# Kernel optimization log

Measured on AMD Instinct MI355X. Metric: run time of the kernel, lower is better.

Reference implementation:

```python
import jax, jax.numpy as jnp
import numpy as np


def setup_inputs() -> dict:
    key = jax.random.key(0)
    k1, k2, k3 = jax.random.split(key, 3)
    B, N = 4096, 1024
    src = jax.random.normal(k1, (B, 3, N), dtype=jnp.float32)
    src_corr = jax.random.normal(k2, (B, 3, N), dtype=jnp.float32)
    weight = jax.random.uniform(k3, (B, 1, N), dtype=jnp.float32)
    return {"src": src, "src_corr": src_corr, "weight": weight}


def reference(src, src_corr, weight):
    # src, src_corr: (B, 3, N); weight: (B, 1, N)
    wsum = weight.sum(axis=2, keepdims=True)                      # (B,1,1)
    src2 = (src * weight).sum(axis=2, keepdims=True) / wsum       # (B,3,1) weighted centroid
    corr2 = (src_corr * weight).sum(axis=2, keepdims=True) / wsum  # (B,3,1)
    src_c = src - src2
    corr_c = src_corr - corr2
    # weighted 3x3 covariance H = (src_c * w) @ corr_c^T
    H = jnp.einsum('bin,bjn->bij', src_c * weight, corr_c)        # (B,3,3)
    u, s, vh = jnp.linalg.svd(H, full_matrices=False)
    v = jnp.swapaxes(vh, -1, -2)                                   # (B,3,3)
    ut = jnp.swapaxes(u, -1, -2)
    det = jnp.linalg.det(v @ ut)                                   # (B,)
    # R = v @ diag(1,1,det) @ u^T  -> scale last column of v by det
    v_adj = v.at[:, :, 2].multiply(det[:, None])
    R = v_adj @ ut                                                 # (B,3,3)
    t = -jnp.matmul(R, src2) + corr2                               # (B,3,1)
    return R, t
```

## Files before the change

kernel.cpp:

```cpp
#include <hip/hip_runtime.h>
#include <math.h>


__global__ __launch_bounds__(256, 3) void wsvd_fused(
    const float* __restrict__ src, const float* __restrict__ corr,
    const float* __restrict__ wgt, float* __restrict__ out, int B)
{
    const int gtid = blockIdx.x * 256 + threadIdx.x;
    const int b = gtid >> 6;
    const int lane = gtid & 63;

    const float4* W4 = reinterpret_cast<const float4*>(wgt  + (size_t)b * 1024);
    const float4* S4 = reinterpret_cast<const float4*>(src  + (size_t)b * 3072);
    const float4* C4 = reinterpret_cast<const float4*>(corr + (size_t)b * 3072);

    float4 wv0 = W4[lane],        wv1 = W4[lane + 64],
           wv2 = W4[lane + 128],  wv3 = W4[lane + 192];
    float4 s00 = S4[lane],        s01 = S4[lane + 64],
           s02 = S4[lane + 128],  s03 = S4[lane + 192];
    float4 s10 = S4[lane + 256],  s11 = S4[lane + 320],
           s12 = S4[lane + 384],  s13 = S4[lane + 448];
    float4 s20 = S4[lane + 512],  s21 = S4[lane + 576],
           s22 = S4[lane + 640],  s23 = S4[lane + 704];
    float4 c00 = C4[lane],        c01 = C4[lane + 64],
           c02 = C4[lane + 128],  c03 = C4[lane + 192];
    float4 c10 = C4[lane + 256],  c11 = C4[lane + 320],
           c12 = C4[lane + 384],  c13 = C4[lane + 448];
    float4 c20 = C4[lane + 512],  c21 = C4[lane + 576],
           c22 = C4[lane + 640],  c23 = C4[lane + 704];

    float wsum = 0.f, ws0 = 0.f, ws1 = 0.f, ws2 = 0.f;
    float wc0 = 0.f, wc1 = 0.f, wc2 = 0.f;
    float m00 = 0.f, m01 = 0.f, m02 = 0.f;
    float m10 = 0.f, m11 = 0.f, m12 = 0.f;
    float m20 = 0.f, m21 = 0.f, m22 = 0.f;

#define PROC1(wv, a0, a1, a2, b0, b1, b2, f) { \
    float w_ = wv.f; \
    float t0 = w_ * a0.f, t1 = w_ * a1.f, t2 = w_ * a2.f; \
    wsum += w_; ws0 += t0; ws1 += t1; ws2 += t2; \
    wc0 += w_ * b0.f; wc1 += w_ * b1.f; wc2 += w_ * b2.f; \
    m00 += t0 * b0.f; m01 += t0 * b1.f; m02 += t0 * b2.f; \
    m10 += t1 * b0.f; m11 += t1 * b1.f; m12 += t1 * b2.f; \
    m20 += t2 * b0.f; m21 += t2 * b1.f; m22 += t2 * b2.f; }
#define PROCV(wv, a0, a1, a2, b0, b1, b2) \
    PROC1(wv, a0, a1, a2, b0, b1, b2, x) \
    PROC1(wv, a0, a1, a2, b0, b1, b2, y) \
    PROC1(wv, a0, a1, a2, b0, b1, b2, z) \
    PROC1(wv, a0, a1, a2, b0, b1, b2, w)

    PROCV(wv0, s00, s10, s20, c00, c10, c20)
    PROCV(wv1, s01, s11, s21, c01, c11, c21)
    PROCV(wv2, s02, s12, s22, c02, c12, c22)
    PROCV(wv3, s03, s13, s23, c03, c13, c23)
#undef PROCV
#undef PROC1

#define BRED(v) { v += __shfl_xor(v, 1); v += __shfl_xor(v, 2); \
                  v += __shfl_xor(v, 4); v += __shfl_xor(v, 8); \
                  v += __shfl_xor(v, 16); v += __shfl_xor(v, 32); }
    BRED(wsum) BRED(ws0) BRED(ws1) BRED(ws2)
    BRED(wc0) BRED(wc1) BRED(wc2)
    BRED(m00) BRED(m01) BRED(m02)
    BRED(m10) BRED(m11) BRED(m12)
    BRED(m20) BRED(m21) BRED(m22)
#undef BRED

    double dwsum = wsum;
    double dws0 = ws0, dws1 = ws1, dws2 = ws2;
    double dwc0 = wc0, dwc1 = wc1, dwc2 = wc2;

    double inv = 1.0 / dwsum;
    double s2x = dws0 * inv, s2y = dws1 * inv, s2z = dws2 * inv;
    double c2x = dwc0 * inv, c2y = dwc1 * inv, c2z = dwc2 * inv;
    double h00 = (double)m00 - dws0 * dwc0 * inv, h01 = (double)m01 - dws0 * dwc1 * inv, h02 = (double)m02 - dws0 * dwc2 * inv;
    double h10 = (double)m10 - dws1 * dwc0 * inv, h11 = (double)m11 - dws1 * dwc1 * inv, h12 = (double)m12 - dws1 * dwc2 * inv;
    double h20 = (double)m20 - dws2 * dwc0 * inv, h21 = (double)m21 - dws2 * dwc1 * inv, h22 = (double)m22 - dws2 * dwc2 * inv;

    double a00 = h00 * h00 + h10 * h10 + h20 * h20;
    double a11 = h01 * h01 + h11 * h11 + h21 * h21;
    double a22 = h02 * h02 + h12 * h12 + h22 * h22;
    double a01 = h00 * h01 + h10 * h11 + h20 * h21;
    double a02 = h00 * h02 + h10 * h12 + h20 * h22;
    double a12 = h01 * h02 + h11 * h12 + h21 * h22;

    double v00 = 1.0, v01 = 0.0, v02 = 0.0;
    double v10 = 0.0, v11 = 1.0, v12 = 0.0;
    double v20 = 0.0, v21 = 0.0, v22 = 1.0;

#define ROT(app, aqq, apq, apr, aqr, vp0, vq0, vp1, vq1, vp2, vq2) { \
    double apq_ = apq; \
    double cc, ss, tt; \
    if (fabs(apq_) > 1e-300) { \
        double tau = (aqq - app) / (2.0 * apq_); \
        tt = copysign(1.0, tau) / (fabs(tau) + sqrt(1.0 + tau * tau)); \
        cc = 1.0 / sqrt(1.0 + tt * tt); ss = tt * cc; \
    } else { tt = 0.0; cc = 1.0; ss = 0.0; } \
    app -= tt * apq_; aqq += tt * apq_; apq = 0.0; \
    { double pr = apr, qr = aqr; apr = cc * pr - ss * qr; aqr = ss * pr + cc * qr; } \
    { double t0_ = vp0; vp0 = cc * t0_ - ss * vq0; vq0 = ss * t0_ + cc * vq0; } \
    { double t0_ = vp1; vp1 = cc * t0_ - ss * vq1; vq1 = ss * t0_ + cc * vq1; } \
    { double t0_ = vp2; vp2 = cc * t0_ - ss * vq2; vq2 = ss * t0_ + cc * vq2; } }

    for (int sweep = 0; sweep < 5; ++sweep) {
        ROT(a00, a11, a01, a02, a12, v00, v01, v10, v11, v20, v21)
        ROT(a00, a22, a02, a01, a12, v00, v02, v10, v12, v20, v22)
        ROT(a11, a22, a12, a01, a02, v01, v02, v11, v12, v21, v22)
    }
#undef ROT

    double l0 = a00, l1 = a11, l2 = a22;
#define CSWAP(li, lj, x0, y0, x1, y1, x2, y2) if (li < lj) { double t_; \
    t_ = li; li = lj; lj = t_; t_ = x0; x0 = y0; y0 = t_; \
    t_ = x1; x1 = y1; y1 = t_; t_ = x2; x2 = y2; y2 = t_; }
    CSWAP(l0, l1, v00, v01, v10, v11, v20, v21)
    CSWAP(l0, l2, v00, v02, v10, v12, v20, v22)
    CSWAP(l1, l2, v01, v02, v11, v12, v21, v22)
#undef CSWAP

    double u0x = h00 * v00 + h01 * v10 + h02 * v20;
    double u0y = h10 * v00 + h11 * v10 + h12 * v20;
    double u0z = h20 * v00 + h21 * v10 + h22 * v20;
    double n0 = sqrt(u0x * u0x + u0y * u0y + u0z * u0z);
    if (n0 > 1e-300) { double r = 1.0 / n0; u0x *= r; u0y *= r; u0z *= r; }
    else { u0x = 1.0; u0y = 0.0; u0z = 0.0; }

    double u1x = h00 * v01 + h01 * v11 + h02 * v21;
    double u1y = h10 * v01 + h11 * v11 + h12 * v21;
    double u1z = h20 * v01 + h21 * v11 + h22 * v21;
    double dp = u0x * u1x + u0y * u1y + u0z * u1z;
    u1x -= dp * u0x; u1y -= dp * u0y; u1z -= dp * u0z;
    double n1 = sqrt(u1x * u1x + u1y * u1y + u1z * u1z);
    if (n1 > 1e-300) { double r = 1.0 / n1; u1x *= r; u1y *= r; u1z *= r; }
    else {
        if (fabs(u0x) < 0.9) { u1x = 0.0; u1y = u0z; u1z = -u0y; }
        else                 { u1x = -u0z; u1y = 0.0; u1z = u0x; }
        double r = 1.0 / sqrt(u1x * u1x + u1y * u1y + u1z * u1z);
        u1x *= r; u1y *= r; u1z *= r;
    }

    double u2x = u0y * u1z - u0z * u1y;
    double u2y = u0z * u1x - u0x * u1z;
    double u2z = u0x * u1y - u0y * u1x;

    double detV = v00 * (v11 * v22 - v12 * v21)
                - v01 * (v10 * v22 - v12 * v20)
                + v02 * (v10 * v21 - v11 * v20);
    double d = (detV >= 0.0) ? 1.0 : -1.0;

    double r00 = v00 * u0x + v01 * u1x + d * v02 * u2x;
    double r01 = v00 * u0y + v01 * u1y + d * v02 * u2y;
    double r02 = v00 * u0z + v01 * u1z + d * v02 * u2z;
    double r10 = v10 * u0x + v11 * u1x + d * v12 * u2x;
    double r11 = v10 * u0y + v11 * u1y + d * v12 * u2y;
    double r12 = v10 * u0z + v11 * u1z + d * v12 * u2z;
    double r20 = v20 * u0x + v21 * u1x + d * v22 * u2x;
    double r21 = v20 * u0y + v21 * u1y + d * v22 * u2y;
    double r22 = v20 * u0z + v21 * u1z + d * v22 * u2z;

    double tx = c2x - (r00 * s2x + r01 * s2y + r02 * s2z);
    double ty = c2y - (r10 * s2x + r11 * s2y + r12 * s2z);
    double tz = c2z - (r20 * s2x + r21 * s2y + r22 * s2z);

    if (lane == 0) {
        float* Ro = out + (size_t)b * 9;
        Ro[0] = (float)r00; Ro[1] = (float)r01; Ro[2] = (float)r02;
        Ro[3] = (float)r10; Ro[4] = (float)r11; Ro[5] = (float)r12;
        Ro[6] = (float)r20; Ro[7] = (float)r21; Ro[8] = (float)r22;
        float* To = out + (size_t)B * 9 + (size_t)b * 3;
        To[0] = (float)tx; To[1] = (float)ty; To[2] = (float)tz;
    }
}

extern "C" void kernel_launch(void* const* d_in, const int* in_sizes, int n_in,
                              void* d_out, int out_size, void* d_ws, size_t ws_size,
                              hipStream_t stream) {
    const float* src  = (const float*)d_in[0];
    const float* corr = (const float*)d_in[1];
    const float* wgt  = (const float*)d_in[2];
    float* out = (float*)d_out;

    const int N = 1024;
    const int B = in_sizes[2] / N;

    wsvd_fused<<<B / 4, 256, 0, stream>>>(src, corr, wgt, out, B);
}
```

Measured before the change: 143.7 us.

## Split each batch across two waves and use fast approximate double rcp/rsqrt

Result: faster. 139.5 us (-2.9%).

```diff
diff --git a/kernel.cpp b/kernel.cpp
--- a/kernel.cpp
+++ b/kernel.cpp
@@ -2,32 +2,42 @@
 #include <math.h>
 
 
-__global__ __launch_bounds__(256, 3) void wsvd_fused(
+__device__ __forceinline__ double drcp(double x) {
+    double r = (double)(1.0f / (float)x);
+    r = r * __fma_rn(-x, r, 2.0);
+    r = r * __fma_rn(-x, r, 2.0);
+    return r;
+}
+__device__ __forceinline__ double drsqrt(double x) {
+    double r = (double)__frsqrt_rn((float)x);
+    r = r * __fma_rn(-0.5 * x * r, r, 1.5);
+    r = r * __fma_rn(-0.5 * x * r, r, 1.5);
+    return r;
+}
+
+__global__ __launch_bounds__(256, 6) void wsvd_fused(
     const float* __restrict__ src, const float* __restrict__ corr,
     const float* __restrict__ wgt, float* __restrict__ out, int B)
 {
-    const int gtid = blockIdx.x * 256 + threadIdx.x;
-    const int b = gtid >> 6;
-    const int lane = gtid & 63;
+    const int wave = threadIdx.x >> 6;
+    const int lane = threadIdx.x & 63;
+    const int b = blockIdx.x * 2 + (wave >> 1);
+    const int h = wave & 1;
 
     const float4* W4 = reinterpret_cast<const float4*>(wgt  + (size_t)b * 1024);
     const float4* S4 = reinterpret_cast<const float4*>(src  + (size_t)b * 3072);
     const float4* C4 = reinterpret_cast<const float4*>(corr + (size_t)b * 3072);
 
-    float4 wv0 = W4[lane],        wv1 = W4[lane + 64],
-           wv2 = W4[lane + 128],  wv3 = W4[lane + 192];
-    float4 s00 = S4[lane],        s01 = S4[lane + 64],
-           s02 = S4[lane + 128],  s03 = S4[lane + 192];
-    float4 s10 = S4[lane + 256],  s11 = S4[lane + 320],
-           s12 = S4[lane + 384],  s13 = S4[lane + 448];
-    float4 s20 = S4[lane + 512],  s21 = S4[lane + 576],
-           s22 = S4[lane + 640],  s23 = S4[lane + 704];
-    float4 c00 = C4[lane],        c01 = C4[lane + 64],
-           c02 = C4[lane + 128],  c03 = C4[lane + 192];
-    float4 c10 = C4[lane + 256],  c11 = C4[lane + 320],
-           c12 = C4[lane + 384],  c13 = C4[lane + 448];
-    float4 c20 = C4[lane + 512],  c21 = C4[lane + 576],
-           c22 = C4[lane + 640],  c23 = C4[lane + 704];
+    const int i0 = h * 128 + lane;
+    const int i1 = i0 + 64;
+
+    float4 wv0 = W4[i0],        wv1 = W4[i1];
+    float4 s00 = S4[i0],        s01 = S4[i1];
+    float4 s10 = S4[i0 + 256],  s11 = S4[i1 + 256];
+    float4 s20 = S4[i0 + 512],  s21 = S4[i1 + 512];
+    float4 c00 = C4[i0],        c01 = C4[i1];
+    float4 c10 = C4[i0 + 256],  c11 = C4[i1 + 256];
+    float4 c20 = C4[i0 + 512],  c21 = C4[i1 + 512];
 
     float wsum = 0.f, ws0 = 0.f, ws1 = 0.f, ws2 = 0.f;
     float wc0 = 0.f, wc1 = 0.f, wc2 = 0.f;
@@ -51,8 +61,6 @@
 
     PROCV(wv0, s00, s10, s20, c00, c10, c20)
     PROCV(wv1, s01, s11, s21, c01, c11, c21)
-    PROCV(wv2, s02, s12, s22, c02, c12, c22)
-    PROCV(wv3, s03, s13, s23, c03, c13, c23)
 #undef PROCV
 #undef PROC1
 
@@ -66,16 +74,32 @@
     BRED(m20) BRED(m21) BRED(m22)
 #undef BRED
 
-    double dwsum = wsum;
-    double dws0 = ws0, dws1 = ws1, dws2 = ws2;
-    double dwc0 = wc0, dwc1 = wc1, dwc2 = wc2;
-
-    double inv = 1.0 / dwsum;
+    __shared__ float sm[4][16];
+    if (lane == 0) {
+        float* o = sm[wave];
+        o[0] = wsum; o[1] = ws0; o[2] = ws1; o[3] = ws2;
+        o[4] = wc0;  o[5] = wc1; o[6] = wc2; o[7] = m00;
+        o[8] = m01;  o[9] = m02; o[10] = m10; o[11] = m11;
+        o[12] = m12; o[13] = m20; o[14] = m21; o[15] = m22;
+    }
+    __syncthreads();
+    if (h != 0) return;
+
+    const float* p0 = sm[wave];
+    const float* p1 = sm[wave + 1];
+    double dwsum = (double)p0[0] + p1[0];
+    double dws0 = (double)p0[1] + p1[1], dws1 = (double)p0[2] + p1[2], dws2 = (double)p0[3] + p1[3];
+    double dwc0 = (double)p0[4] + p1[4], dwc1 = (double)p0[5] + p1[5], dwc2 = (double)p0[6] + p1[6];
+    double dm00 = (double)p0[7] + p1[7], dm01 = (double)p0[8] + p1[8], dm02 = (double)p0[9] + p1[9];
+    double dm10 = (double)p0[10] + p1[10], dm11 = (double)p0[11] + p1[11], dm12 = (double)p0[12] + p1[12];
+    double dm20 = (double)p0[13] + p1[13], dm21 = (double)p0[14] + p1[14], dm22 = (double)p0[15] + p1[15];
+
+    double inv = drcp(dwsum);
     double s2x = dws0 * inv, s2y = dws1 * inv, s2z = dws2 * inv;
     double c2x = dwc0 * inv, c2y = dwc1 * inv, c2z = dwc2 * inv;
-    double h00 = (double)m00 - dws0 * dwc0 * inv, h01 = (double)m01 - dws0 * dwc1 * inv, h02 = (double)m02 - dws0 * dwc2 * inv;
-    double h10 = (double)m10 - dws1 * dwc0 * inv, h11 = (double)m11 - dws1 * dwc1 * inv, h12 = (double)m12 - dws1 * dwc2 * inv;
-    double h20 = (double)m20 - dws2 * dwc0 * inv, h21 = (double)m21 - dws2 * dwc1 * inv, h22 = (double)m22 - dws2 * dwc2 * inv;
+    double h00 = dm00 - dws0 * dwc0 * inv, h01 = dm01 - dws0 * dwc1 * inv, h02 = dm02 - dws0 * dwc2 * inv;
+    double h10 = dm10 - dws1 * dwc0 * inv, h11 = dm11 - dws1 * dwc1 * inv, h12 = dm12 - dws1 * dwc2 * inv;
+    double h20 = dm20 - dws2 * dwc0 * inv, h21 = dm21 - dws2 * dwc1 * inv, h22 = dm22 - dws2 * dwc2 * inv;
 
     double a00 = h00 * h00 + h10 * h10 + h20 * h20;
     double a11 = h01 * h01 + h11 * h11 + h21 * h21;
@@ -90,17 +114,18 @@
 
 #define ROT(app, aqq, apq, apr, aqr, vp0, vq0, vp1, vq1, vp2, vq2) { \
     double apq_ = apq; \
-    double cc, ss, tt; \
-    if (fabs(apq_) > 1e-300) { \
-        double tau = (aqq - app) / (2.0 * apq_); \
-        tt = copysign(1.0, tau) / (fabs(tau) + sqrt(1.0 + tau * tau)); \
-        cc = 1.0 / sqrt(1.0 + tt * tt); ss = tt * cc; \
-    } else { tt = 0.0; cc = 1.0; ss = 0.0; } \
-    app -= tt * apq_; aqq += tt * apq_; apq = 0.0; \
-    { double pr = apr, qr = aqr; apr = cc * pr - ss * qr; aqr = ss * pr + cc * qr; } \
-    { double t0_ = vp0; vp0 = cc * t0_ - ss * vq0; vq0 = ss * t0_ + cc * vq0; } \
-    { double t0_ = vp1; vp1 = cc * t0_ - ss * vq1; vq1 = ss * t0_ + cc * vq1; } \
-    { double t0_ = vp2; vp2 = cc * t0_ - ss * vq2; vq2 = ss * t0_ + cc * vq2; } }
+    if (fabs(apq_) > fmax(1e-35, 1e-15 * (fabs(app) + fabs(aqq)))) { \
+        double tau = (aqq - app) * 0.5 * drcp(apq_); \
+        double t2_ = 1.0 + tau * tau; \
+        double sq_ = t2_ * drsqrt(t2_); \
+        double tt = copysign(1.0, tau) * drcp(fabs(tau) + sq_); \
+        double cc = drsqrt(1.0 + tt * tt); \
+        double ss = tt * cc; \
+        app -= tt * apq_; aqq += tt * apq_; apq = 0.0; \
+        { double pr = apr, qr = aqr; apr = cc * pr - ss * qr; aqr = ss * pr + cc * qr; } \
+        { double t0_ = vp0; vp0 = cc * t0_ - ss * vq0; vq0 = ss * t0_ + cc * vq0; } \
+        { double t0_ = vp1; vp1 = cc * t0_ - ss * vq1; vq1 = ss * t0_ + cc * vq1; } \
+        { double t0_ = vp2; vp2 = cc * t0_ - ss * vq2; vq2 = ss * t0_ + cc * vq2; } } }
 
     for (int sweep = 0; sweep < 5; ++sweep) {
         ROT(a00, a11, a01, a02, a12, v00, v01, v10, v11, v20, v21)
@@ -121,8 +146,8 @@
     double u0x = h00 * v00 + h01 * v10 + h02 * v20;
     double u0y = h10 * v00 + h11 * v10 + h12 * v20;
     double u0z = h20 * v00 + h21 * v10 + h22 * v20;
-    double n0 = sqrt(u0x * u0x + u0y * u0y + u0z * u0z);
-    if (n0 > 1e-300) { double r = 1.0 / n0; u0x *= r; u0y *= r; u0z *= r; }
+    double n0sq = u0x * u0x + u0y * u0y + u0z * u0z;
+    if (n0sq > 1e-30) { double r = drsqrt(n0sq); u0x *= r; u0y *= r; u0z *= r; }
     else { u0x = 1.0; u0y = 0.0; u0z = 0.0; }
 
     double u1x = h00 * v01 + h01 * v11 + h02 * v21;
@@ -130,12 +155,12 @@
     double u1z = h20 * v01 + h21 * v11 + h22 * v21;
     double dp = u0x * u1x + u0y * u1y + u0z * u1z;
     u1x -= dp * u0x; u1y -= dp * u0y; u1z -= dp * u0z;
-    double n1 = sqrt(u1x * u1x + u1y * u1y + u1z * u1z);
-    if (n1 > 1e-300) { double r = 1.0 / n1; u1x *= r; u1y *= r; u1z *= r; }
+    double n1sq = u1x * u1x + u1y * u1y + u1z * u1z;
+    if (n1sq > 1e-30) { double r = drsqrt(n1sq); u1x *= r; u1y *= r; u1z *= r; }
     else {
         if (fabs(u0x) < 0.9) { u1x = 0.0; u1y = u0z; u1z = -u0y; }
         else                 { u1x = -u0z; u1y = 0.0; u1z = u0x; }
-        double r = 1.0 / sqrt(u1x * u1x + u1y * u1y + u1z * u1z);
+        double r = drsqrt(u1x * u1x + u1y * u1y + u1z * u1z);
         u1x *= r; u1y *= r; u1z *= r;
     }
 
@@ -183,5 +208,5 @@
     const int N = 1024;
     const int B = in_sizes[2] / N;
 
-    wsvd_fused<<<B / 4, 256, 0, stream>>>(src, corr, wgt, out, B);
-}
+    wsvd_fused<<<B / 2, 256, 0, stream>>>(src, corr, wgt, out, B);
+}
```
